# Performance work log

Measured on AMD Instinct MI355X. Metric: run time of the kernel, lower is better.

The kernel has to match this reference:

```python
import jax, jax.numpy as jnp
from jax import lax
import numpy as np

RADIUS = 0.2   # ball-query radius (module init arg)
NSAMPLE = 32   # gather_size
STRIDE = 4     # npoint = ceil(N / STRIDE)


def setup_inputs() -> dict:
    key = jax.random.key(0)
    k1, k2, k3 = jax.random.split(key, 3)
    points = jax.random.uniform(k1, (4, 8192, 3), jnp.float32)      # (B,N,3) in unit cube
    features = jax.random.normal(k2, (4, 8192, 64), jnp.float32)    # (B,N,C)
    # Conv2d(in=C+3, out=128, kernel=(1, NSAMPLE), bias=False) weight
    weight = jax.random.normal(k3, (128, 67, 1, 32), jnp.float32) * 0.02
    return {"points": points, "features": features, "weight": weight}


def fps(xyz, npoint):
    """Furthest point sampling. xyz: (B,N,3) -> inds (B,npoint) int32."""
    B, N, _ = xyz.shape
    start = jnp.zeros((B,), jnp.int32)          # standard FPS starts at index 0
    dist0 = jnp.full((B, N), 1e10, xyz.dtype)

    def body(carry, _):
        dist, last = carry
        last_xyz = jnp.take_along_axis(xyz, last[:, None, None], axis=1)  # (B,1,3)
        d = jnp.sum((xyz - last_xyz) ** 2, axis=-1)                        # (B,N)
        dist = jnp.minimum(dist, d)
        nxt = jnp.argmax(dist, axis=-1).astype(jnp.int32)
        return (dist, nxt), nxt

    (_, _), rest = lax.scan(body, (dist0, start), None, length=npoint - 1)
    return jnp.concatenate([start[None, :], rest], axis=0).T  # (B,npoint)


def ball_query(xyz, new_xyz, radius, nsample):
    """For each center, first `nsample` point indices within radius, padded with
    the first valid index (pointnet2 semantics). Returns (B,npoint,nsample)."""
    N = xyz.shape[1]
    d2 = jnp.sum((new_xyz[:, :, None, :] - xyz[:, None, :, :]) ** 2, axis=-1)  # (B,npoint,N)
    cand = jnp.where(d2 < radius * radius, jnp.arange(N, dtype=jnp.int32), N)
    neg, _ = lax.top_k(-cand, nsample)   # smallest nsample indices, in order
    idx = -neg
    first = idx[..., :1]                 # center itself is always in-ball -> valid
    return jnp.where(idx == N, first, idx)


def _forward(points, features, weight):
    B, N, _ = points.shape
    npoint = (N + STRIDE - 1) // STRIDE
    inds = fps(points, npoint)                                        # (B,npoint)
    new_xyz = jnp.take_along_axis(points, inds[..., None], axis=1)    # (B,npoint,3)
    idx = ball_query(points, new_xyz, RADIUS, NSAMPLE)                # (B,npoint,nsample)

    gather = lambda v: jax.vmap(lambda a, i: a[i])(v, idx)            # (B,npoint,nsample,*)
    g_xyz = gather(points) - new_xyz[:, :, None, :]                   # relative coords
    g_feat = gather(features)
    g = jnp.concatenate([g_xyz, g_feat], axis=-1)                     # (B,npoint,nsample,3+C)

    # Conv2d with kernel (1,nsample): contract over channel + neighbor axes.
    conv = jnp.einsum("bpsc,ocs->bpo", g, weight[:, :, 0, :])         # (B,npoint,Cout)
    return new_xyz, conv


def reference(points, features, weight):
    return _forward(points, features, weight)
```

## Files before the change

### kernel.cpp

```cpp
#include <hip/hip_runtime.h>

#define BATCH   4
#define NPTS    8192
#define NPOINT  2048
#define NSAMPLE 32
#define NCH     67
#define NOUT    128
#define NP      4
#define FPS_T   256
#define KPT     (NPTS / FPS_T)
#define NWAVE   (FPS_T / 64)

#define DPP_ROW_SHR1   0x111
#define DPP_ROW_SHR2   0x112
#define DPP_ROW_SHR4   0x114
#define DPP_ROW_SHR8   0x118
#define DPP_ROW_BCAST15 0x142
#define DPP_ROW_BCAST31 0x143

#define DPP_MAX_HOP(key, ctrl)                                                 \
    {                                                                          \
        int _lo = (int)(unsigned)(key);                                        \
        int _hi = (int)(unsigned)((key) >> 32);                                \
        int _olo = __builtin_amdgcn_update_dpp(0, _lo, (ctrl), 0xF, 0xF, true);\
        int _ohi = __builtin_amdgcn_update_dpp(0, _hi, (ctrl), 0xF, 0xF, true);\
        unsigned long long _o =                                                \
            ((unsigned long long)(unsigned)_ohi << 32) | (unsigned)_olo;       \
        if (_o > (key)) (key) = _o;                                            \
    }

__global__ __launch_bounds__(FPS_T, 1)
__attribute__((amdgpu_waves_per_eu(1, 1)))
void fps_kernel(const float* __restrict__ points, float* __restrict__ new_xyz)
{
#pragma clang fp contract(off)
    const int b = blockIdx.x;
    const int t = threadIdx.x;
    const float* pts = points + (size_t)b * NPTS * 3;

    __shared__ float px[NPTS], py[NPTS], pz[NPTS];
    __shared__ unsigned long long pk[2][NWAVE];

    float x[KPT], y[KPT], z[KPT], dist[KPT];
#pragma unroll
    for (int k = 0; k < KPT; ++k) {
        const int i = (k << 8) + t;
        const float xx = pts[3 * i + 0];
        const float yy = pts[3 * i + 1];
        const float zz = pts[3 * i + 2];
        x[k] = xx; y[k] = yy; z[k] = zz;
        dist[k] = 10000000000.0f;
        px[i] = xx; py[i] = yy; pz[i] = zz;
    }

    float cx = pts[0], cy = pts[1], cz = pts[2];
    if (t == 0) {
        float* o = new_xyz + (size_t)b * NPOINT * 3;
        o[0] = cx; o[1] = cy; o[2] = cz;
    }
    const int lane = t & 63;
    const int w    = t >> 6;
    __syncthreads();

    for (int it = 1; it < NPOINT; ++it) {
        float bv; int bk = 0;
        {
            float dx = x[0] - cx, dy = y[0] - cy, dz = z[0] - cz;
            float d  = ((dx * dx) + (dy * dy)) + (dz * dz);
            float dk = fminf(dist[0], d);
            dist[0] = dk; bv = dk;
        }
#pragma unroll
        for (int k = 1; k < KPT; ++k) {
            float dx = x[k] - cx, dy = y[k] - cy, dz = z[k] - cz;
            float d  = ((dx * dx) + (dy * dy)) + (dz * dz);
            float dk = fminf(dist[k], d);
            dist[k] = dk;
            if (dk > bv) { bv = dk; bk = k; }
        }
        const int bi = (bk << 8) + t;
        unsigned long long key =
            ((unsigned long long)__float_as_uint(bv) << 32) | (unsigned)(~bi);

        DPP_MAX_HOP(key, DPP_ROW_SHR1);
        DPP_MAX_HOP(key, DPP_ROW_SHR2);
        DPP_MAX_HOP(key, DPP_ROW_SHR4);
        DPP_MAX_HOP(key, DPP_ROW_SHR8);
        DPP_MAX_HOP(key, DPP_ROW_BCAST15);
        DPP_MAX_HOP(key, DPP_ROW_BCAST31);

        const int par = it & 1;
        if (lane == 63) pk[par][w] = key;
        __syncthreads();

        unsigned long long k0 = pk[par][0], k1 = pk[par][1];
        unsigned long long k2 = pk[par][2], k3 = pk[par][3];
        if (k1 > k0) k0 = k1;
        if (k3 > k2) k2 = k3;
        if (k2 > k0) k0 = k2;
        const int idx = ~(int)(unsigned)k0;
        cx = px[idx]; cy = py[idx]; cz = pz[idx];
        if (t == 0) {
            float* o = new_xyz + ((size_t)b * NPOINT + it) * 3;
            o[0] = cx; o[1] = cy; o[2] = cz;
        }
    }
}

__global__ __launch_bounds__(256) void ballq_kernel(
    const float* __restrict__ points, const float* __restrict__ new_xyz,
    int* __restrict__ ballidx)
{
#pragma clang fp contract(off)
    const int wid  = (int)((blockIdx.x * 256 + threadIdx.x) >> 6);
    const int lane = threadIdx.x & 63;
    const int b = wid / NPOINT;
    const float* ctr = new_xyz + (size_t)wid * 3;
    const float cx = ctr[0], cy = ctr[1], cz = ctr[2];
    const float* pts = points + (size_t)b * NPTS * 3;
    int* out = ballidx + (size_t)wid * NSAMPLE;
    const float r2 = (float)(0.2 * 0.2);

    int cnt = 0;
    int first = 0;
    bool havefirst = false;
    for (int base = 0; base < NPTS && cnt < NSAMPLE; base += 64) {
        const int j = base + lane;
        float dx = pts[3 * j + 0] - cx;
        float dy = pts[3 * j + 1] - cy;
        float dz = pts[3 * j + 2] - cz;
        float d2 = ((dx * dx) + (dy * dy)) + (dz * dz);
        const bool in = d2 < r2;
        unsigned long long m = __ballot(in);
        if (in) {
            int pos = cnt + __popcll(m & ((1ull << lane) - 1ull));
            if (pos < NSAMPLE) out[pos] = j;
        }
        if (!havefirst && m != 0ull) {
            first = base + (__ffsll((long long)m) - 1);
            havefirst = true;
        }
        cnt += __popcll(m);
    }
    if (lane >= cnt && lane < NSAMPLE) out[lane] = first;
}

__global__ __launch_bounds__(128) void conv_kernel(
    const float* __restrict__ points, const float* __restrict__ features,
    const float* __restrict__ weight, const float* __restrict__ new_xyz,
    const int* __restrict__ ballidx, float* __restrict__ conv_out)
{
    __shared__ float g[NP][NCH][NSAMPLE];
    const int t = threadIdx.x;
    const int bp0 = blockIdx.x * NP;
    const int b = bp0 / NPOINT;
    const float* pts = points + (size_t)b * NPTS * 3;
    const float* fts = features + (size_t)b * NPTS * 64;

    {
        const int p = t >> 5;
        const int s = t & 31;
        const int ci = bp0 + p;
        const int j = ballidx[(size_t)ci * NSAMPLE + s];
        const float* ctr = new_xyz + (size_t)ci * 3;
        const float* pj = pts + 3 * j;
        g[p][0][s] = pj[0] - ctr[0];
        g[p][1][s] = pj[1] - ctr[1];
        g[p][2][s] = pj[2] - ctr[2];
        const float4* fj = (const float4*)(fts + (size_t)j * 64);
#pragma unroll
        for (int c4 = 0; c4 < 16; ++c4) {
            float4 v = fj[c4];
            g[p][3 + 4 * c4 + 0][s] = v.x;
            g[p][3 + 4 * c4 + 1][s] = v.y;
            g[p][3 + 4 * c4 + 2][s] = v.z;
            g[p][3 + 4 * c4 + 3][s] = v.w;
        }
    }
    __syncthreads();

    const int o = t;
    float acc0 = 0.f, acc1 = 0.f, acc2 = 0.f, acc3 = 0.f;
    const float* wr = weight + (size_t)o * NCH * NSAMPLE;
    for (int c = 0; c < NCH; ++c) {
        const float4* w4 = (const float4*)(wr + c * NSAMPLE);
#pragma unroll
        for (int s4 = 0; s4 < 8; ++s4) {
            float4 wv = w4[s4];
            float4 g0 = *(const float4*)&g[0][c][s4 * 4];
            float4 g1 = *(const float4*)&g[1][c][s4 * 4];
            float4 g2 = *(const float4*)&g[2][c][s4 * 4];
            float4 g3 = *(const float4*)&g[3][c][s4 * 4];
            acc0 += g0.x * wv.x + g0.y * wv.y + g0.z * wv.z + g0.w * wv.w;
            acc1 += g1.x * wv.x + g1.y * wv.y + g1.z * wv.z + g1.w * wv.w;
            acc2 += g2.x * wv.x + g2.y * wv.y + g2.z * wv.z + g2.w * wv.w;
            acc3 += g3.x * wv.x + g3.y * wv.y + g3.z * wv.z + g3.w * wv.w;
        }
    }
    float* outp = conv_out + (size_t)bp0 * NOUT;
    outp[0 * NOUT + o] = acc0;
    outp[1 * NOUT + o] = acc1;
    outp[2 * NOUT + o] = acc2;
    outp[3 * NOUT + o] = acc3;
}

extern "C" void kernel_launch(void* const* d_in, const int* in_sizes, int n_in,
                              void* d_out, int out_size, void* d_ws, size_t ws_size,
                              hipStream_t stream)
{
    const float* points   = (const float*)d_in[0];
    const float* features = (const float*)d_in[1];
    const float* weight   = (const float*)d_in[2];

    float* new_xyz = (float*)d_out;
    float* conv    = (float*)d_out + (size_t)BATCH * NPOINT * 3;

    int* ballidx = (int*)d_ws;

    fps_kernel<<<BATCH, FPS_T, 0, stream>>>(points, new_xyz);
    ballq_kernel<<<(BATCH * NPOINT * 64) / 256, 256, 0, stream>>>(points, new_xyz, ballidx);
    conv_kernel<<<(BATCH * NPOINT) / NP, 128, 0, stream>>>(points, features, weight, new_xyz, ballidx, conv);
}
```

Before: 2.220 ms.

## Bucket points into spatial grid cells to prune FPS distance updates

Sorts each batch's points into a 256-cell bounding-box grid in shared memory and keeps a per-cell max-distance key. Each FPS iteration skips cells whose box is farther from the new center than the cell's current max distance, because their min-distances cannot change. Only the surviving cells are scanned, one cell per wave, and their keys are reduced. This trades the full 8192-point update per iteration for list building, extra barriers, shared-memory atomics and load imbalance when points are clustered. Per-cell length is capped at 2047, which would miss points in very dense cells.

```diff
diff --git a/kernel.cpp b/kernel.cpp
--- a/kernel.cpp
+++ b/kernel.cpp
@@ -8,13 +8,13 @@
 #define NOUT    128
 #define NP      4
 #define FPS_T   256
+#define NWAVE   (FPS_T / 64)
 #define KPT     (NPTS / FPS_T)
-#define NWAVE   (FPS_T / 64)
-
-#define DPP_ROW_SHR1   0x111
-#define DPP_ROW_SHR2   0x112
-#define DPP_ROW_SHR4   0x114
-#define DPP_ROW_SHR8   0x118
+
+#define DPP_ROW_SHR1    0x111
+#define DPP_ROW_SHR2    0x112
+#define DPP_ROW_SHR4    0x114
+#define DPP_ROW_SHR8    0x118
 #define DPP_ROW_BCAST15 0x142
 #define DPP_ROW_BCAST31 0x143
 
@@ -29,77 +29,172 @@
         if (_o > (key)) (key) = _o;                                            \
     }
 
-__global__ __launch_bounds__(FPS_T, 1)
-__attribute__((amdgpu_waves_per_eu(1, 1)))
-void fps_kernel(const float* __restrict__ points, float* __restrict__ new_xyz)
+#define DPP_REDUCE_MAX(key)            \
+    DPP_MAX_HOP(key, DPP_ROW_SHR1);    \
+    DPP_MAX_HOP(key, DPP_ROW_SHR2);    \
+    DPP_MAX_HOP(key, DPP_ROW_SHR4);    \
+    DPP_MAX_HOP(key, DPP_ROW_SHR8);    \
+    DPP_MAX_HOP(key, DPP_ROW_BCAST15); \
+    DPP_MAX_HOP(key, DPP_ROW_BCAST31);
+
+__global__ __launch_bounds__(FPS_T) void fps_kernel(
+    const float* __restrict__ points, float* __restrict__ new_xyz)
 {
 #pragma clang fp contract(off)
-    const int b = blockIdx.x;
-    const int t = threadIdx.x;
+    const int b    = blockIdx.x;
+    const int t    = threadIdx.x;
+    const int lane = t & 63;
+    const int w    = t >> 6;
     const float* pts = points + (size_t)b * NPTS * 3;
 
-    __shared__ float px[NPTS], py[NPTS], pz[NPTS];
+    __shared__ float4 pxyzd[NPTS];
+    __shared__ unsigned short orig16[NPTS];
+    __shared__ unsigned long long key_g[FPS_T];
+    __shared__ int start[FPS_T + 1];
+    __shared__ int cursor[FPS_T];
+    __shared__ unsigned list[FPS_T];
     __shared__ unsigned long long pk[2][NWAVE];
-
-    float x[KPT], y[KPT], z[KPT], dist[KPT];
-#pragma unroll
+    __shared__ int cnt2[2];
+    __shared__ float bbr[6][NWAVE];
+
+    float mnx = 1e30f, mny = 1e30f, mnz = 1e30f;
+    float mxx = -1e30f, mxy = -1e30f, mxz = -1e30f;
     for (int k = 0; k < KPT; ++k) {
         const int i = (k << 8) + t;
-        const float xx = pts[3 * i + 0];
-        const float yy = pts[3 * i + 1];
-        const float zz = pts[3 * i + 2];
-        x[k] = xx; y[k] = yy; z[k] = zz;
-        dist[k] = 10000000000.0f;
-        px[i] = xx; py[i] = yy; pz[i] = zz;
-    }
+        float xx = pts[3 * i], yy = pts[3 * i + 1], zz = pts[3 * i + 2];
+        mnx = fminf(mnx, xx); mxx = fmaxf(mxx, xx);
+        mny = fminf(mny, yy); mxy = fmaxf(mxy, yy);
+        mnz = fminf(mnz, zz); mxz = fmaxf(mxz, zz);
+    }
+#pragma unroll
+    for (int off = 32; off >= 1; off >>= 1) {
+        mnx = fminf(mnx, __shfl_down(mnx, off));
+        mny = fminf(mny, __shfl_down(mny, off));
+        mnz = fminf(mnz, __shfl_down(mnz, off));
+        mxx = fmaxf(mxx, __shfl_down(mxx, off));
+        mxy = fmaxf(mxy, __shfl_down(mxy, off));
+        mxz = fmaxf(mxz, __shfl_down(mxz, off));
+    }
+    if (lane == 0) {
+        bbr[0][w] = mnx; bbr[1][w] = mny; bbr[2][w] = mnz;
+        bbr[3][w] = mxx; bbr[4][w] = mxy; bbr[5][w] = mxz;
+    }
+    cursor[t] = 0;
+    if (t < 2) cnt2[t] = 0;
+    __syncthreads();
+    mnx = fminf(fminf(bbr[0][0], bbr[0][1]), fminf(bbr[0][2], bbr[0][3]));
+    mny = fminf(fminf(bbr[1][0], bbr[1][1]), fminf(bbr[1][2], bbr[1][3]));
+    mnz = fminf(fminf(bbr[2][0], bbr[2][1]), fminf(bbr[2][2], bbr[2][3]));
+    mxx = fmaxf(fmaxf(bbr[3][0], bbr[3][1]), fmaxf(bbr[3][2], bbr[3][3]));
+    mxy = fmaxf(fmaxf(bbr[4][0], bbr[4][1]), fmaxf(bbr[4][2], bbr[4][3]));
+    mxz = fmaxf(fmaxf(bbr[5][0], bbr[5][1]), fmaxf(bbr[5][2], bbr[5][3]));
+    const float rx = mxx - mnx, ry = mxy - mny, rz = mxz - mnz;
+    const float sclx = (rx > 0.f) ? 8.0f / rx : 0.f;
+    const float scly = (ry > 0.f) ? 8.0f / ry : 0.f;
+    const float sclz = (rz > 0.f) ? 4.0f / rz : 0.f;
+
+    for (int k = 0; k < KPT; ++k) {
+        const int i = (k << 8) + t;
+        float xx = pts[3 * i], yy = pts[3 * i + 1], zz = pts[3 * i + 2];
+        int cxi = min(7, max(0, (int)((xx - mnx) * sclx)));
+        int cyi = min(7, max(0, (int)((yy - mny) * scly)));
+        int czi = min(3, max(0, (int)((zz - mnz) * sclz)));
+        atomicAdd(&cursor[cxi | (cyi << 3) | (czi << 6)], 1);
+    }
+    __syncthreads();
+    if (t == 0) {
+        int acc = 0;
+        for (int g = 0; g < FPS_T; ++g) { start[g] = acc; acc += cursor[g]; }
+        start[FPS_T] = acc;
+    }
+    __syncthreads();
+    const int s0_reg  = start[t];
+    int       len_reg = start[t + 1] - s0_reg;
+    if (len_reg > 2047) len_reg = 2047;
+    cursor[t] = s0_reg;
+    __syncthreads();
+
+    for (int k = 0; k < KPT; ++k) {
+        const int i = (k << 8) + t;
+        float xx = pts[3 * i], yy = pts[3 * i + 1], zz = pts[3 * i + 2];
+        int cxi = min(7, max(0, (int)((xx - mnx) * sclx)));
+        int cyi = min(7, max(0, (int)((yy - mny) * scly)));
+        int czi = min(3, max(0, (int)((zz - mnz) * sclz)));
+        int slot = atomicAdd(&cursor[cxi | (cyi << 3) | (czi << 6)], 1);
+        pxyzd[slot] = make_float4(xx, yy, zz, 10000000000.0f);
+        orig16[slot] = (unsigned short)i;
+    }
+
+    const float cwx = rx * 0.125f, cwy = ry * 0.125f, cwz = rz * 0.25f;
+    const float bxl = mnx + (float)(t & 7) * cwx,        bxh = bxl + cwx;
+    const float byl = mny + (float)((t >> 3) & 7) * cwy, byh = byl + cwy;
+    const float bzl = mnz + (float)(t >> 6) * cwz,       bzh = bzl + cwz;
 
     float cx = pts[0], cy = pts[1], cz = pts[2];
     if (t == 0) {
         float* o = new_xyz + (size_t)b * NPOINT * 3;
         o[0] = cx; o[1] = cy; o[2] = cz;
     }
-    const int lane = t & 63;
-    const int w    = t >> 6;
+    unsigned long long kk =
+        ((unsigned long long)__float_as_uint(10000000000.0f) << 32);
     __syncthreads();
 
     for (int it = 1; it < NPOINT; ++it) {
-        float bv; int bk = 0;
-        {
-            float dx = x[0] - cx, dy = y[0] - cy, dz = z[0] - cz;
-            float d  = ((dx * dx) + (dy * dy)) + (dz * dz);
-            float dk = fminf(dist[0], d);
-            dist[0] = dk; bv = dk;
-        }
-#pragma unroll
-        for (int k = 1; k < KPT; ++k) {
-            float dx = x[k] - cx, dy = y[k] - cy, dz = z[k] - cz;
-            float d  = ((dx * dx) + (dy * dy)) + (dz * dz);
-            float dk = fminf(dist[k], d);
-            dist[k] = dk;
-            if (dk > bv) { bv = dk; bk = k; }
-        }
-        const int bi = (bk << 8) + t;
-        unsigned long long key =
-            ((unsigned long long)__float_as_uint(bv) << 32) | (unsigned)(~bi);
-
-        DPP_MAX_HOP(key, DPP_ROW_SHR1);
-        DPP_MAX_HOP(key, DPP_ROW_SHR2);
-        DPP_MAX_HOP(key, DPP_ROW_SHR4);
-        DPP_MAX_HOP(key, DPP_ROW_SHR8);
-        DPP_MAX_HOP(key, DPP_ROW_BCAST15);
-        DPP_MAX_HOP(key, DPP_ROW_BCAST31);
-
         const int par = it & 1;
-        if (lane == 63) pk[par][w] = key;
+        float ddx = fmaxf(fmaxf(bxl - cx, cx - bxh), 0.0f);
+        float ddy = fmaxf(fmaxf(byl - cy, cy - byh), 0.0f);
+        float ddz = fmaxf(fmaxf(bzl - cz, cz - bzh), 0.0f);
+        float dmin2 = ddx * ddx + ddy * ddy + ddz * ddz;
+        float ub = __uint_as_float((unsigned)(kk >> 32));
+        bool scan = dmin2 < ub * 1.0001f + 1e-5f;
+        unsigned long long m = __ballot(scan);
+        int base;
+        if (lane == 0) base = atomicAdd(&cnt2[par], __popcll(m));
+        base = __builtin_amdgcn_readfirstlane(base);
+        if (scan) {
+            int pos = base + __popcll(m & ((1ull << lane) - 1ull));
+            list[pos] = (unsigned)((t << 24) | (s0_reg << 11) | len_reg);
+        }
+        if (t == 0) cnt2[1 - par] = 0;
         __syncthreads();
-
+        const int nb = cnt2[par];
+
+        for (int li = w; li < nb; li += NWAVE) {
+            unsigned e = list[li];
+            int g  = e >> 24;
+            int s0 = (e >> 11) & 0x1FFF;
+            int ln = e & 0x7FF;
+            unsigned long long bk = 0;
+            for (int jo = lane; jo < ln; jo += 64) {
+                int j = s0 + jo;
+                float4 pd = pxyzd[j];
+                float dx = pd.x - cx, dy = pd.y - cy, dz = pd.z - cz;
+                float d  = ((dx * dx) + (dy * dy)) + (dz * dz);
+                float nd = fminf(pd.w, d);
+                pxyzd[j].w = nd;
+                unsigned long long kkey =
+                    ((unsigned long long)__float_as_uint(nd) << 32)
+                  | ((unsigned)(8191 - (int)orig16[j]) << 13) | (unsigned)j;
+                if (kkey > bk) bk = kkey;
+            }
+            DPP_REDUCE_MAX(bk);
+            if (lane == 63) key_g[g] = bk;
+        }
+        __syncthreads();
+
+        kk = key_g[t];
+        unsigned long long r = kk;
+        DPP_REDUCE_MAX(r);
+        if (lane == 63) pk[par][w] = r;
+        __syncthreads();
         unsigned long long k0 = pk[par][0], k1 = pk[par][1];
         unsigned long long k2 = pk[par][2], k3 = pk[par][3];
         if (k1 > k0) k0 = k1;
         if (k3 > k2) k2 = k3;
         if (k2 > k0) k0 = k2;
-        const int idx = ~(int)(unsigned)k0;
-        cx = px[idx]; cy = py[idx]; cz = pz[idx];
+        const int slot = (int)(k0 & 0x1FFF);
+        float4 wc = pxyzd[slot];
+        cx = wc.x; cy = wc.y; cz = wc.z;
         if (t == 0) {
             float* o = new_xyz + ((size_t)b * NPOINT + it) * 3;
             o[0] = cx; o[1] = cy; o[2] = cz;
```

New measurement: 2.854 ms. 1.29x slower.
